# Performance work log

Measured on AMD Instinct MI355X. Metric: run time of the kernel, lower is better.

## Reference

```python
import jax, jax.numpy as jnp
import numpy as np

N, B, L, C, H = 16384, 16, 32, 256, 8
DH = C // H
K_STATIC = 16   # k_max for L=32 (L>20 -> min(16, L//2))
K_MIN = 8       # int(0.25*L)
LN_EPS = 1e-5


def _ln(x, g, b):
    m = x.mean(-1, keepdims=True)
    v = ((x - m) ** 2).mean(-1, keepdims=True)
    return (x - m) / jnp.sqrt(v + LN_EPS) * g + b


def setup_inputs() -> dict:
    key = jax.random.key(0)
    ks = jax.random.split(key, 12)
    s = 1.0 / np.sqrt(C)
    f32 = jnp.float32
    return {
        'vision_features': jax.random.normal(ks[0], (N, B, C), dtype=f32),
        'text_features': jax.random.normal(ks[1], (L, B, C), dtype=f32),
        'vp_w': jax.random.normal(ks[2], (C, C), dtype=f32) * s,
        'vp_b': jnp.zeros((C,), f32),
        'tp_w': jax.random.normal(ks[3], (C, C), dtype=f32) * s,
        'tp_b': jnp.zeros((C,), f32),
        'in_proj_w': jax.random.normal(ks[4], (3 * C, C), dtype=f32) * s,
        'in_proj_b': jnp.zeros((3 * C,), f32),
        'w1': jax.random.normal(ks[5], (C, C), dtype=f32) * s,
        'b1': jnp.zeros((C,), f32),
        'g1': jnp.ones((C,), f32),
        'be1': jnp.zeros((C,), f32),
        'w2': jax.random.normal(ks[6], (C // 2, C), dtype=f32) * s,
        'b2': jnp.zeros((C // 2,), f32),
        'g2': jnp.ones((C // 2,), f32),
        'be2': jnp.zeros((C // 2,), f32),
        'w3': jax.random.normal(ks[7], (1, C // 2), dtype=f32) * s,
        'b3': jnp.zeros((1,), f32),
        'k_weight': jnp.asarray(np.log(0.4 / 0.6), f32),
        'alpha_coarse': jnp.asarray(np.log(0.72 / 0.28), f32),
        'alpha_fine': jnp.asarray(np.log(0.82 / 0.18), f32),
    }


def reference(vision_features, text_features, vp_w, vp_b, tp_w, tp_b,
              in_proj_w, in_proj_b, w1, b1, g1, be1, w2, b2, g2, be2,
              w3, b3, k_weight, alpha_coarse, alpha_fine):
    # projections (torch Linear: y = x W^T + b)
    vision_proj = vision_features @ vp_w.T + vp_b  # [N,B,C]
    text_proj = text_features @ tp_w.T + tp_b      # [L,B,C]

    # nn.MultiheadAttention attention weights, averaged over heads
    qp = vision_proj @ in_proj_w[:C].T + in_proj_b[:C]
    kp = text_proj @ in_proj_w[C:2 * C].T + in_proj_b[C:2 * C]
    q = qp.reshape(N, B, H, DH)
    k = kp.reshape(L, B, H, DH)
    scores = jnp.einsum('nbhd,lbhd->bhnl', q, k) / np.sqrt(DH)
    attn = jax.nn.softmax(scores, axis=-1).mean(axis=1)  # [B,N,L]

    # data-dependent k_top per batch (unbiased variance over L, mean over N)
    mu = attn.mean(axis=-1, keepdims=True)
    var = ((attn - mu) ** 2).sum(axis=-1) / (L - 1)       # [B,N]
    attn_variance = var.mean(axis=1)                      # [B]
    k_ws = jax.nn.sigmoid(k_weight)
    ratio = jnp.clip(k_ws * (1.0 + attn_variance * 0.5), 0.25, 0.6)
    k_base = jnp.maximum(1, jnp.floor(L * ratio).astype(jnp.int32))
    k_top = jnp.maximum(K_MIN, jnp.minimum(jnp.minimum(K_STATIC, k_base), L))  # [B]

    # variable-k top-k via static K_STATIC + mask
    top = -jnp.sort(-attn, axis=-1)[..., :K_STATIC]       # [B,N,K]
    mask = jnp.arange(K_STATIC)[None, None, :] < k_top[:, None, None]
    logits = jnp.where(mask, top, -jnp.inf)
    w = jax.nn.softmax(logits, axis=-1)
    similarity_score = jnp.sum(jnp.where(mask, top * w, 0.0), axis=-1)  # [B,N]

    # importance MLP on raw vision features (dropout off at inference)
    h = jax.nn.relu(_ln(vision_features @ w1.T + b1, g1, be1))
    h = jax.nn.relu(_ln(h @ w2.T + b2, g2, be2))
    feature_importance = jax.nn.sigmoid(h @ w3.T + b3)[..., 0]  # [N,B]
    feature_importance = feature_importance.T                    # [B,N]

    def minmax(x):
        lo = x.min(axis=1, keepdims=True)
        rng = x.max(axis=1, keepdims=True) - lo
        return jnp.where(rng > 0, (x - lo) / rng, 0.0)

    sim_norm = minmax(similarity_score)
    imp_norm = minmax(feature_importance)

    alpha = (jax.nn.sigmoid(alpha_coarse) + jax.nn.sigmoid(alpha_fine)) / 2.0
    importance = alpha * sim_norm + (1.0 - alpha) * imp_norm  # [B,N]
    return importance.T  # [N,B]
```

## Files before the change

kernel.cpp:

```cpp
#include <hip/hip_runtime.h>
#include <hip/hip_bf16.h>

typedef _Float16 f16;
typedef _Float16 half8 __attribute__((ext_vector_type(8)));
typedef _Float16 half4 __attribute__((ext_vector_type(4)));
typedef float f32x4 __attribute__((ext_vector_type(4)));

typedef const __attribute__((address_space(1))) void gvoid;
typedef __attribute__((address_space(3))) void lvoid;
#define GLOAD16(src, dst) __builtin_amdgcn_global_load_lds((gvoid*)(src), (lvoid*)(dst), 16, 0, 0)

#define WQV_OFF   0u
#define WKT_OFF   262144u
#define KP_OFF    524288u
#define W2S_OFF   1048576u
#define SBIAS_OFF 3145728u
#define BQV_OFF   3162112u
#define BKT_OFF   3163136u
#define W1H_OFF   3164160u
#define W2H_OFF   3295232u
#define VARP_OFF  3360768u
#define SMM_OFF   3377280u
#define FMM_OFF   3377408u
#define CAND_OFF  3377664u
#define FI_OFF    12814848u
#define SIM_OFF   13863424u
#define XS_OFF    14912000u
#define XS_BYTES  134217728ull

__device__ __forceinline__ float sigm(float x) { return 1.f / (1.f + __expf(-x)); }
__device__ __forceinline__ unsigned fmap(float f) {
  unsigned u = __float_as_uint(f);
  return (u & 0x80000000u) ? ~u : (u | 0x80000000u);
}
__device__ __forceinline__ float funmap(unsigned u) {
  unsigned b = (u & 0x80000000u) ? (u & 0x7FFFFFFFu) : ~u;
  return __uint_as_float(b);
}

__global__ void k_p1(const float* __restrict__ ipw, const float* __restrict__ ipb,
                     const float* __restrict__ vp_w, const float* __restrict__ vp_b,
                     const float* __restrict__ tp_w, const float* __restrict__ tp_b,
                     float* __restrict__ Wqv, float* __restrict__ Wkt,
                     float* __restrict__ bqv, float* __restrict__ bkt,
                     unsigned* __restrict__ simMM, unsigned* __restrict__ fiMM) {
  int tx = threadIdx.x, ty = threadIdx.y;
  int bz = blockIdx.z;
  if (bz == 2) {
    if (blockIdx.x || blockIdx.y) return;
    if (ty == 0 && tx < 16) {
      simMM[tx * 2] = 0xFFFFFFFFu; simMM[tx * 2 + 1] = 0u;
      fiMM[tx * 2] = 0xFFFFFFFFu;  fiMM[tx * 2 + 1] = 0u;
    }
    int j = ty * 16 + tx;
    float s1 = 0.f, s2 = 0.f;
    for (int k = 0; k < 256; ++k) {
      s1 += ipw[j * 256 + k] * vp_b[k];
      s2 += ipw[65536 + j * 256 + k] * tp_b[k];
    }
    bqv[j] = s1 + ipb[j];
    bkt[j] = s2 + ipb[256 + j];
    return;
  }
  const float* A = ipw + (bz ? 65536 : 0);
  const float* B = bz ? tp_w : vp_w;
  float* O = bz ? Wkt : Wqv;
  __shared__ float As[16][16], Bs[16][17];
  int row = blockIdx.y * 16 + ty, col = blockIdx.x * 16 + tx;
  float s = 0.f;
  for (int tt = 0; tt < 16; ++tt) {
    As[ty][tx] = A[row * 256 + tt * 16 + tx];
    Bs[ty][tx] = B[(tt * 16 + ty) * 256 + col];
    __syncthreads();
#pragma unroll
    for (int k = 0; k < 16; ++k) s += As[ty][k] * Bs[k][tx];
    __syncthreads();
  }
  O[row * 256 + col] = s;
}

__global__ void k_conv(const float* __restrict__ w1, const float* __restrict__ w2,
                       char* __restrict__ W1g, char* __restrict__ W2g) {
  int i = blockIdx.x * 256 + threadIdx.x;
  if (i < 65536) {
    int o = i >> 8, c = i & 255;
    *(f16*)(W1g + (c >> 6) * 32768 + o * 128 + (((c & 63) << 1) ^ ((o & 7) << 4))) = (f16)w1[i];
  } else if (i < 98304) {
    int i2 = i - 65536;
    int o = i2 >> 8, c = i2 & 255;
    *(f16*)(W2g + (c >> 6) * 16384 + o * 128 + (((c & 63) << 1) ^ ((o & 7) << 4))) = (f16)w2[i2];
  }
}

__global__ void __launch_bounds__(256) k_tr(const float* __restrict__ X,
                                            char* __restrict__ XS) {
  int g0 = blockIdx.x * 256 + threadIdx.x;
#pragma unroll 4
  for (int i = 0; i < 16; ++i) {
    int G = g0 + i * 524288;
    int cg = G & 31;
    int nb = G >> 5;
    int b = nb & 15;
    int n = nb >> 4;
    f32x4 a0 = *(const f32x4*)(X + (size_t)G * 8);
    f32x4 a1 = *(const f32x4*)(X + (size_t)G * 8 + 4);
    half8 h;
#pragma unroll
    for (int j = 0; j < 4; ++j) { h[j] = (f16)a0[j]; h[4 + j] = (f16)a1[j]; }
    unsigned off = (unsigned)((cg >> 3) * 128 + (((cg & 7) << 4) ^ ((n & 7) << 4)));
    *(half8*)(XS + ((size_t)b * 16384 + n) * 512 + off) = h;
  }
}

__global__ void k_p2(const float* __restrict__ T, const float* __restrict__ Wkt,
                     const float* __restrict__ bkt, float* __restrict__ kp) {
  __shared__ float As[16][16], Ws[16][17];
  int tx = threadIdx.x, ty = threadIdx.y;
  int lb = blockIdx.y * 16 + ty;
  int i = blockIdx.x * 16 + tx;
  float s = 0.f;
  for (int tt = 0; tt < 16; ++tt) {
    As[ty][tx] = T[(size_t)lb * 256 + tt * 16 + tx];
    Ws[ty][tx] = Wkt[(size_t)(blockIdx.x * 16 + ty) * 256 + tt * 16 + tx];
    __syncthreads();
#pragma unroll
    for (int k = 0; k < 16; ++k) s += As[ty][k] * Ws[tx][k];
    __syncthreads();
  }
  kp[(size_t)lb * 256 + i] = s + bkt[i];
}

__global__ void k_p3(const float* __restrict__ kp, const float* __restrict__ Wqv,
                     const float* __restrict__ bqv, char* __restrict__ W2sg,
                     float* __restrict__ sbias) {
  const float SC = 0.17677669529663687f;
  int b = blockIdx.z, jt = blockIdx.y, ct = blockIdx.x;
  int ty = threadIdx.y, tx = threadIdx.x;
  int j2 = jt * 16 + ty, c = ct * 16 + tx;
  int h = j2 >> 5, l = j2 & 31;
  const float* kr = kp + (size_t)(l * 16 + b) * 256 + h * 32;
  const float* wq = Wqv + (size_t)h * 32 * 256 + c;
  float s = 0.f;
#pragma unroll
  for (int d = 0; d < 32; ++d) s += kr[d] * wq[(size_t)d * 256];
  *(f16*)(W2sg + (size_t)b * 131072 + (c >> 6) * 32768 + j2 * 128 +
          (((c & 63) << 1) ^ ((j2 & 7) << 4))) = (f16)(s * SC);
  if (ct == 0 && tx == 0) {
    float sb = 0.f;
#pragma unroll
    for (int d = 0; d < 32; ++d) sb += kr[d] * bqv[h * 32 + d];
    sbias[b * 256 + j2] = sb * SC;
  }
}

template <int CONT>
__global__ void __launch_bounds__(256, 3) k_sc(
    const float* __restrict__ X, const char* __restrict__ XSg,
    const char* __restrict__ W2sg, const float* __restrict__ sbias,
    float* __restrict__ cand, float* __restrict__ varpart) {
  __shared__ __align__(16) char smem[40960];
  const int b = blockIdx.y;
  const int bx = blockIdx.x;
  const int n0 = bx * 64;
  const int t = threadIdx.x;
  const int w = t >> 6;
  const int lane = t & 63;
  const int ln = lane & 15, kg = lane >> 4;
  char* AT = smem;
  char* BT = smem + 8192;
  const char* XSb = XSg + ((size_t)b * 16384 + n0) * 512;
  const char* Wb = W2sg + (size_t)b * 131072;

  auto issueA = [&](int kt) {
    if constexpr (CONT) {
      const char* src = XSb + (size_t)(w * 16 + (lane >> 3)) * 512 + kt * 128 + ((lane & 7) << 4);
      GLOAD16(src, AT + w * 2048);
      GLOAD16(src + 8 * 512, AT + w * 2048 + 1024);
    } else {
      int row = t >> 2, cq = t & 3;
      const float* Xr = X + ((size_t)(n0 + row) * 16 + b) * 256 + kt * 64 + cq * 16;
      f32x4 a0 = *(const f32x4*)(Xr), a1 = *(const f32x4*)(Xr + 4);
      f32x4 a2 = *(const f32x4*)(Xr + 8), a3 = *(const f32x4*)(Xr + 12);
      half8 h0, h1;
#pragma unroll
      for (int i = 0; i < 4; ++i) {
        h0[i] = (f16)a0[i]; h0[4 + i] = (f16)a1[i];
        h1[i] = (f16)a2[i]; h1[4 + i] = (f16)a3[i];
      }
      unsigned sw = (unsigned)((row & 7) << 4);
      *(half8*)(AT + ((unsigned)(row * 128 + cq * 32) ^ sw)) = h0;
      *(half8*)(AT + ((unsigned)(row * 128 + cq * 32 + 16) ^ sw)) = h1;
    }
  };
  auto issueB = [&](int kt) {
    const char* src = Wb + kt * 32768 + w * 8192 + (lane << 4);
    char* dst = BT + w * 8192;
#pragma unroll
    for (int i = 0; i < 8; ++i) GLOAD16(src + i * 1024, dst + i * 1024);
  };

  f32x4 acc[4][4];
#pragma unroll
  for (int q = 0; q < 4; ++q)
#pragma unroll
    for (int ni = 0; ni < 4; ++ni)
#pragma unroll
      for (int i = 0; i < 4; ++i) acc[q][ni][i] = 0.f;

  issueA(0); issueB(0);
  __syncthreads();
#pragma unroll
  for (int kt = 0; kt < 4; ++kt) {
    half8 av[4][2], bv[4][2];
#pragma unroll
    for (int q = 0; q < 4; ++q) {
      int o = w * 64 + q * 16 + ln;
      unsigned sw = (unsigned)((o & 7) << 4);
#pragma unroll
      for (int mi = 0; mi < 2; ++mi)
        av[q][mi] = *(const half8*)(BT + o * 128 + ((unsigned)(mi * 64 + kg * 16) ^ sw));
    }
#pragma unroll
    for (int ni = 0; ni < 4; ++ni) {
      int n = ni * 16 + ln;
      unsigned sw = (unsigned)((n & 7) << 4);
#pragma unroll
      for (int mi = 0; mi < 2; ++mi)
        bv[ni][mi] = *(const half8*)(AT + n * 128 + ((unsigned)(mi * 64 + kg * 16) ^ sw));
    }
#pragma unroll
    for (int mi = 0; mi < 2; ++mi)
#pragma unroll
      for (int q = 0; q < 4; ++q)
#pragma unroll
        for (int ni = 0; ni < 4; ++ni)
          acc[q][ni] = __builtin_amdgcn_mfma_f32_16x16x32_f16(av[q][mi], bv[ni][mi], acc[q][ni], 0, 0, 0);
    __syncthreads();
    if (kt < 3) { issueA(kt + 1); issueB(kt + 1); __syncthreads(); }
  }

  {
    f32x4 sb[4];
#pragma unroll
    for (int q = 0; q < 4; ++q)
      sb[q] = *(const f32x4*)(sbias + b * 256 + (w * 4 + q) * 16 + kg * 4);
    float vm[4][2][4];
#pragma unroll
    for (int ni = 0; ni < 4; ++ni)
#pragma unroll
      for (int qq = 0; qq < 2; ++qq)
#pragma unroll
        for (int r = 0; r < 4; ++r) vm[ni][qq][r] = 0.f;
#pragma unroll
    for (int hh = 0; hh < 2; ++hh)
#pragma unroll
      for (int ni = 0; ni < 4; ++ni) {
        float x[2][4];
        float mx = -1e30f;
#pragma unroll
        for (int qq = 0; qq < 2; ++qq)
#pragma unroll
          for (int r = 0; r < 4; ++r) {
            x[qq][r] = acc[hh * 2 + qq][ni][r] + sb[hh * 2 + qq][r];
            mx = fmaxf(mx, x[qq][r]);
          }
        mx = fmaxf(mx, __shfl_xor(mx, 16, 64));
        mx = fmaxf(mx, __shfl_xor(mx, 32, 64));
        float S = 0.f;
#pragma unroll
        for (int qq = 0; qq < 2; ++qq)
#pragma unroll
          for (int r = 0; r < 4; ++r) { x[qq][r] = __expf(x[qq][r] - mx); S += x[qq][r]; }
        S += __shfl_xor(S, 16, 64);
        S += __shfl_xor(S, 32, 64);
        float inv = 0.125f / S;
#pragma unroll
        for (int qq = 0; qq < 2; ++qq)
#pragma unroll
          for (int r = 0; r < 4; ++r) vm[ni][qq][r] += x[qq][r] * inv;
      }
    float* slice = (float*)(smem + 8192) + w * 2048;
#pragma unroll
    for (int ni = 0; ni < 4; ++ni)
#pragma unroll
      for (int qq = 0; qq < 2; ++qq)
#pragma unroll
        for (int r = 0; r < 4; ++r)
          slice[(qq * 16 + kg * 4 + r) * 64 + ni * 16 + ln] = vm[ni][qq][r];
  }
  __syncthreads();

  if (w == 0) {
    const float* sl = (const float*)(smem + 8192);
    float v[32];
#pragma unroll
    for (int l = 0; l < 32; ++l)
      v[l] = sl[l * 64 + lane] + sl[2048 + l * 64 + lane] +
             sl[4096 + l * 64 + lane] + sl[6144 + l * 64 + lane];
    float s2 = 0.f;
#pragma unroll
    for (int l = 0; l < 32; ++l) s2 += v[l] * v[l];
    float vr = (s2 - (1.f / 32.f)) * (1.f / 31.f);
#pragma unroll
    for (int m = 1; m < 64; m <<= 1) vr += __shfl_xor(vr, m, 64);
    if (lane == 0) varpart[b * 256 + bx] = vr;
#pragma unroll
    for (int k = 2; k <= 32; k <<= 1) {
#pragma unroll
      for (int j = k >> 1; j > 0; j >>= 1) {
#pragma unroll
        for (int i = 0; i < 32; ++i) {
          int l = i ^ j;
          if (l > i) {
            float a = v[i], c = v[l];
            float hi = fmaxf(a, c), lo = fminf(a, c);
            bool up = ((i & k) == 0);
            v[i] = up ? hi : lo;
            v[l] = up ? lo : hi;
          }
        }
      }
    }
    float m0 = v[0], se = 0.f, te = 0.f;
    float cn[9];
#pragma unroll
    for (int i = 0; i < 16; ++i) {
      float e = __expf(v[i] - m0);
      se += e; te += v[i] * e;
      if (i >= 7) cn[i - 7] = te / se;
    }
#pragma unroll
    for (int i = 0; i < 9; ++i)
      cand[(size_t)i * 262144 + (size_t)b * 16384 + n0 + lane] = cn[i];
  }
}

template <int CONT>
__global__ void __launch_bounds__(256, 3) k_mlp(
    const float* __restrict__ X, const char* __restrict__ XSg,
    const char* __restrict__ W1g, const char* __restrict__ W2g,
    const float* __restrict__ b1, const float* __restrict__ g1, const float* __restrict__ be1,
    const float* __restrict__ b2, const float* __restrict__ g2, const float* __restrict__ be2,
    const float* __restrict__ w3, const float* __restrict__ b3,
    float* __restrict__ fi) {
  __shared__ __align__(16) char smem[49152];
  __shared__ float pSQ[2][64][5];
  __shared__ float pM[64], pR[64];
  const int b = blockIdx.y;
  const int bx = blockIdx.x;
  const int n0 = bx * 64;
  const int t = threadIdx.x;
  const int w = t >> 6;
  const int lane = t & 63;
  const int ln = lane & 15, kg = lane >> 4;
  char* AT = smem;
  char* BT = smem + 8192;
  char* H1 = smem;
  char* W2T = smem + 32768;
  const char* XSb = XSg + ((size_t)b * 16384 + n0) * 512;

  auto issueA = [&](int kt) {
    if constexpr (CONT) {
      const char* src = XSb + (size_t)(w * 16 + (lane >> 3)) * 512 + kt * 128 + ((lane & 7) << 4);
      GLOAD16(src, AT + w * 2048);
      GLOAD16(src + 8 * 512, AT + w * 2048 + 1024);
    } else {
      int row = t >> 2, cq = t & 3;
      const float* Xr = X + ((size_t)(n0 + row) * 16 + b) * 256 + kt * 64 + cq * 16;
      f32x4 a0 = *(const f32x4*)(Xr), a1 = *(const f32x4*)(Xr + 4);
      f32x4 a2 = *(const f32x4*)(Xr + 8), a3 = *(const f32x4*)(Xr + 12);
      half8 h0, h1;
#pragma unroll
      for (int i = 0; i < 4; ++i) {
        h0[i] = (f16)a0[i]; h0[4 + i] = (f16)a1[i];
        h1[i] = (f16)a2[i]; h1[4 + i] = (f16)a3[i];
      }
      unsigned sw = (unsigned)((row & 7) << 4);
      *(half8*)(AT + ((unsigned)(row * 128 + cq * 32) ^ sw)) = h0;
      *(half8*)(AT + ((unsigned)(row * 128 + cq * 32 + 16) ^ sw)) = h1;
    }
  };
  auto issueB1 = [&](int kt) {
    const char* src = W1g + kt * 32768 + w * 8192 + (lane << 4);
    char* dst = BT + w * 8192;
#pragma unroll
    for (int i = 0; i < 8; ++i) GLOAD16(src + i * 1024, dst + i * 1024);
  };
  auto issueW2 = [&](int kt) {
    const char* src = W2g + kt * 16384 + w * 4096 + (lane << 4);
    char* dst = W2T + w * 4096;
    GLOAD16(src, dst);
    GLOAD16(src + 1024, dst + 1024);
    GLOAD16(src + 2048, dst + 2048);
    GLOAD16(src + 3072, dst + 3072);
  };

  f32x4 acc[4][4];
#pragma unroll
  for (int q = 0; q < 4; ++q)
#pragma unroll
    for (int ni = 0; ni < 4; ++ni)
#pragma unroll
      for (int i = 0; i < 4; ++i) acc[q][ni][i] = 0.f;

  issueA(0); issueB1(0);
  __syncthreads();
#pragma unroll
  for (int kt = 0; kt < 4; ++kt) {
    half8 av[4][2], bv[4][2];
#pragma unroll
    for (int q = 0; q < 4; ++q) {
      int o = w * 64 + q * 16 + ln;
      unsigned sw = (unsigned)((o & 7) << 4);
#pragma unroll
      for (int mi = 0; mi < 2; ++mi)
        av[q][mi] = *(const half8*)(BT + o * 128 + ((unsigned)(mi * 64 + kg * 16) ^ sw));
    }
#pragma unroll
    for (int ni = 0; ni < 4; ++ni) {
      int n = ni * 16 + ln;
      unsigned sw = (unsigned)((n & 7) << 4);
#pragma unroll
      for (int mi = 0; mi < 2; ++mi)
        bv[ni][mi] = *(const half8*)(AT + n * 128 + ((unsigned)(mi * 64 + kg * 16) ^ sw));
    }
#pragma unroll
    for (int mi = 0; mi < 2; ++mi)
#pragma unroll
      for (int q = 0; q < 4; ++q)
#pragma unroll
        for (int ni = 0; ni < 4; ++ni)
          acc[q][ni] = __builtin_amdgcn_mfma_f32_16x16x32_f16(av[q][mi], bv[ni][mi], acc[q][ni], 0, 0, 0);
    __syncthreads();
    if (kt < 3) { issueA(kt + 1); issueB1(kt + 1); __syncthreads(); }
  }
  issueW2(0);

  {
    f32x4 b1v[4];
#pragma unroll
    for (int q = 0; q < 4; ++q)
      b1v[q] = *(const f32x4*)(b1 + (w * 4 + q) * 16 + kg * 4);
#pragma unroll
    for (int ni = 0; ni < 4; ++ni) {
      float s = 0.f, qq = 0.f;
#pragma unroll
      for (int q = 0; q < 4; ++q)
#pragma unroll
        for (int r = 0; r < 4; ++r) {
          float v = acc[q][ni][r] + b1v[q][r];
          acc[q][ni][r] = v;
          s += v; qq += v * v;
        }
      s += __shfl_xor(s, 16, 64); s += __shfl_xor(s, 32, 64);
      qq += __shfl_xor(qq, 16, 64); qq += __shfl_xor(qq, 32, 64);
      if (kg == 0) { int n = ni * 16 + ln; pSQ[0][n][w] = s; pSQ[1][n][w] = qq; }
    }
  }
  __syncthreads();
  if (t < 64) {
    float s = pSQ[0][t][0] + pSQ[0][t][1] + pSQ[0][t][2] + pSQ[0][t][3];
    float q = pSQ[1][t][0] + pSQ[1][t][1] + pSQ[1][t][2] + pSQ[1][t][3];
    float mean = s * (1.f / 256.f);
    float var = q * (1.f / 256.f) - mean * mean;
    pM[t] = mean;
    pR[t] = rsqrtf(var + 1e-5f);
  }
  __syncthreads();

  {
    f32x4 g1v[4], e1v[4];
#pragma unroll
    for (int q = 0; q < 4; ++q) {
      g1v[q] = *(const f32x4*)(g1 + (w * 4 + q) * 16 + kg * 4);
      e1v[q] = *(const f32x4*)(be1 + (w * 4 + q) * 16 + kg * 4);
    }
#pragma unroll
    for (int ni = 0; ni < 4; ++ni) {
      int n = ni * 16 + ln;
      float mean = pM[n], rstd = pR[n];
      unsigned sw = (unsigned)((n & 7) << 4);
#pragma unroll
      for (int q = 0; q < 4; ++q) {
        half4 hv;
#pragma unroll
        for (int r = 0; r < 4; ++r) {
          float y = (acc[q][ni][r] - mean) * rstd * g1v[q][r] + e1v[q][r];
          hv[r] = (f16)fmaxf(y, 0.f);
        }
        *(half4*)(H1 + ((unsigned)(n * 512 + (w * 4 + q) * 32 + kg * 8) ^ sw)) = hv;
      }
    }
  }
  __syncthreads();

  f32x4 acc2[2][4];
#pragma unroll
  for (int oi = 0; oi < 2; ++oi)
#pragma unroll
    for (int ni = 0; ni < 4; ++ni)
#pragma unroll
      for (int i = 0; i < 4; ++i) acc2[oi][ni][i] = 0.f;
#pragma unroll
  for (int kt = 0; kt < 4; ++kt) {
    half8 a2[2][2], bv[4][2];
#pragma unroll
    for (int oi = 0; oi < 2; ++oi) {
      int o2 = w * 32 + oi * 16 + ln;
      unsigned sw = (unsigned)((o2 & 7) << 4);
#pragma unroll
      for (int mi = 0; mi < 2; ++mi)
        a2[oi][mi] = *(const half8*)(W2T + o2 * 128 + ((unsigned)(mi * 64 + kg * 16) ^ sw));
    }
#pragma unroll
    for (int ni = 0; ni < 4; ++ni) {
      int n = ni * 16 + ln;
      unsigned sw = (unsigned)((n & 7) << 4);
#pragma unroll
      for (int mi = 0; mi < 2; ++mi)
        bv[ni][mi] = *(const half8*)(H1 + n * 512 + kt * 128 + ((unsigned)(mi * 64 + kg * 16) ^ sw));
    }
#pragma unroll
    for (int mi = 0; mi < 2; ++mi)
#pragma unroll
      for (int oi = 0; oi < 2; ++oi)
#pragma unroll
        for (int ni = 0; ni < 4; ++ni)
          acc2[oi][ni] = __builtin_amdgcn_mfma_f32_16x16x32_f16(a2[oi][mi], bv[ni][mi], acc2[oi][ni], 0, 0, 0);
    __syncthreads();
    if (kt < 3) { issueW2(kt + 1); __syncthreads(); }
  }

  {
    f32x4 b2v[2], g2v[2], e2v[2], w3v[2];
#pragma unroll
    for (int oi = 0; oi < 2; ++oi) {
      b2v[oi] = *(const f32x4*)(b2 + (w * 2 + oi) * 16 + kg * 4);
      g2v[oi] = *(const f32x4*)(g2 + (w * 2 + oi) * 16 + kg * 4);
      e2v[oi] = *(const f32x4*)(be2 + (w * 2 + oi) * 16 + kg * 4);
      w3v[oi] = *(const f32x4*)(w3 + (w * 2 + oi) * 16 + kg * 4);
    }
#pragma unroll
    for (int ni = 0; ni < 4; ++ni) {
      float s = 0.f, q = 0.f;
#pragma unroll
      for (int oi = 0; oi < 2; ++oi)
#pragma unroll
        for (int r = 0; r < 4; ++r) {
          float v = acc2[oi][ni][r] + b2v[oi][r];
          acc2[oi][ni][r] = v;
          s += v; q += v * v;
        }
      s += __shfl_xor(s, 16, 64); s += __shfl_xor(s, 32, 64);
      q += __shfl_xor(q, 16, 64); q += __shfl_xor(q, 32, 64);
      if (kg == 0) { int n = ni * 16 + ln; pSQ[0][n][w] = s; pSQ[1][n][w] = q; }
    }
    __syncthreads();
    if (t < 64) {
      float s = pSQ[0][t][0] + pSQ[0][t][1] + pSQ[0][t][2] + pSQ[0][t][3];
      float q = pSQ[1][t][0] + pSQ[1][t][1] + pSQ[1][t][2] + pSQ[1][t][3];
      float mean = s * (1.f / 128.f);
      float var = q * (1.f / 128.f) - mean * mean;
      pM[t] = mean;
      pR[t] = rsqrtf(var + 1e-5f);
    }
    __syncthreads();
#pragma unroll
    for (int ni = 0; ni < 4; ++ni) {
      int n = ni * 16 + ln;
      float mean = pM[n], rstd = pR[n];
      float a3 = 0.f;
#pragma unroll
      for (int oi = 0; oi < 2; ++oi)
#pragma unroll
        for (int r = 0; r < 4; ++r) {
          float y = (acc2[oi][ni][r] - mean) * rstd * g2v[oi][r] + e2v[oi][r];
          a3 += fmaxf(y, 0.f) * w3v[oi][r];
        }
      a3 += __shfl_xor(a3, 16, 64);
      a3 += __shfl_xor(a3, 32, 64);
      if (kg == 0) pSQ[0][n][w] = a3;
    }
    __syncthreads();
    if (t < 64) {
      float z = pSQ[0][t][0] + pSQ[0][t][1] + pSQ[0][t][2] + pSQ[0][t][3] + b3[0];
      fi[(size_t)b * 16384 + n0 + t] = sigm(z);
    }
  }
}

__global__ void __launch_bounds__(256) k_g4(
    const float* __restrict__ cand, const float* __restrict__ fi,
    const float* __restrict__ varpart, const float* __restrict__ kw,
    float* __restrict__ sim, unsigned* __restrict__ simMM, unsigned* __restrict__ fiMM) {
  __shared__ float red[4][4];
  __shared__ int kS;
  int b = blockIdx.x >> 6;
  if (threadIdx.x < 64) {
    float s = 0.f;
#pragma unroll
    for (int i = 0; i < 4; ++i) s += varpart[b * 256 + threadIdx.x + i * 64];
#pragma unroll
    for (int m = 1; m < 64; m <<= 1) s += __shfl_xor(s, m, 64);
    if (threadIdx.x == 0) {
      float var = s * (1.f / 16384.f);
      float kws = sigm(kw[0]);
      float ratio = fminf(fmaxf(kws * (1.f + var * 0.5f), 0.25f), 0.6f);
      int kb = (int)floorf(32.f * ratio);
      if (kb < 1) kb = 1;
      int kt = kb < 16 ? kb : 16;
      if (kt < 8) kt = 8;
      kS = kt;
    }
  }
  __syncthreads();
  int k = kS;
  int n = (blockIdx.x & 63) * 256 + threadIdx.x;
  size_t idx = (size_t)b * 16384 + n;
  float sv = cand[(size_t)(k - 8) * 262144 + idx];
  sim[idx] = sv;
  float fv = fi[idx];
  float sn = sv, sx = sv, fn = fv, fx = fv;
#pragma unroll
  for (int m = 1; m < 64; m <<= 1) {
    sn = fminf(sn, __shfl_xor(sn, m, 64));
    sx = fmaxf(sx, __shfl_xor(sx, m, 64));
    fn = fminf(fn, __shfl_xor(fn, m, 64));
    fx = fmaxf(fx, __shfl_xor(fx, m, 64));
  }
  int wv = threadIdx.x >> 6;
  if ((threadIdx.x & 63) == 0) { red[0][wv] = sn; red[1][wv] = sx; red[2][wv] = fn; red[3][wv] = fx; }
  __syncthreads();
  if (threadIdx.x == 0) {
    float a = red[0][0], c = red[1][0], d = red[2][0], e = red[3][0];
#pragma unroll
    for (int i = 1; i < 4; ++i) {
      a = fminf(a, red[0][i]); c = fmaxf(c, red[1][i]);
      d = fminf(d, red[2][i]); e = fmaxf(e, red[3][i]);
    }
    atomicMin(&simMM[b * 2 + 0], fmap(a));
    atomicMax(&simMM[b * 2 + 1], fmap(c));
    atomicMin(&fiMM[b * 2 + 0], fmap(d));
    atomicMax(&fiMM[b * 2 + 1], fmap(e));
  }
}

__global__ void __launch_bounds__(256) k_g5(
    const float* __restrict__ sim, const float* __restrict__ fi,
    const unsigned* __restrict__ simMM, const unsigned* __restrict__ fiMM,
    const float* __restrict__ ac, const float* __restrict__ af,
    float* __restrict__ out) {
  __shared__ float ls[256][17], lf[256][17];
  __shared__ float sMin[16], sInv[16], fMin[16], fInv[16];
  int t = threadIdx.x;
  int n0 = blockIdx.x * 256;
  if (t < 16) {
    float lo = funmap(simMM[t * 2]), hi = funmap(simMM[t * 2 + 1]);
    float r = hi - lo;
    sMin[t] = lo; sInv[t] = (r > 0.f) ? 1.f / r : 0.f;
    lo = funmap(fiMM[t * 2]); hi = funmap(fiMM[t * 2 + 1]);
    r = hi - lo;
    fMin[t] = lo; fInv[t] = (r > 0.f) ? 1.f / r : 0.f;
  }
#pragma unroll
  for (int i = 0; i < 16; ++i) {
    ls[t][i] = sim[(size_t)i * 16384 + n0 + t];
    lf[t][i] = fi[(size_t)i * 16384 + n0 + t];
  }
  __syncthreads();
  float alpha = 0.5f * (sigm(ac[0]) + sigm(af[0]));
  float o[16];
#pragma unroll
  for (int b = 0; b < 16; ++b) {
    float s = (ls[t][b] - sMin[b]) * sInv[b];
    float f = (lf[t][b] - fMin[b]) * fInv[b];
    o[b] = alpha * s + (1.f - alpha) * f;
  }
  float* op = out + (size_t)(n0 + t) * 16;
#pragma unroll
  for (int i = 0; i < 4; ++i) {
    f32x4 v;
    v[0] = o[i * 4]; v[1] = o[i * 4 + 1]; v[2] = o[i * 4 + 2]; v[3] = o[i * 4 + 3];
    *(f32x4*)(op + i * 4) = v;
  }
}

extern "C" void kernel_launch(void* const* d_in, const int* in_sizes, int n_in,
                              void* d_out, int out_size, void* d_ws, size_t ws_size,
                              hipStream_t stream) {
  const float* X    = (const float*)d_in[0];
  const float* T    = (const float*)d_in[1];
  const float* vp_w = (const float*)d_in[2];
  const float* vp_b = (const float*)d_in[3];
  const float* tp_w = (const float*)d_in[4];
  const float* tp_b = (const float*)d_in[5];
  const float* ipw  = (const float*)d_in[6];
  const float* ipb  = (const float*)d_in[7];
  const float* w1   = (const float*)d_in[8];
  const float* b1   = (const float*)d_in[9];
  const float* g1   = (const float*)d_in[10];
  const float* be1  = (const float*)d_in[11];
  const float* w2   = (const float*)d_in[12];
  const float* b2   = (const float*)d_in[13];
  const float* g2   = (const float*)d_in[14];
  const float* be2  = (const float*)d_in[15];
  const float* w3   = (const float*)d_in[16];
  const float* b3   = (const float*)d_in[17];
  const float* kw   = (const float*)d_in[18];
  const float* ac   = (const float*)d_in[19];
  const float* af   = (const float*)d_in[20];
  char* ws = (char*)d_ws;
  float* Wqv = (float*)(ws + WQV_OFF);
  float* Wkt = (float*)(ws + WKT_OFF);
  float* kp = (float*)(ws + KP_OFF);
  char* W2sg = ws + W2S_OFF;
  float* sbias = (float*)(ws + SBIAS_OFF);
  float* bqv = (float*)(ws + BQV_OFF);
  float* bkt = (float*)(ws + BKT_OFF);
  char* W1g = ws + W1H_OFF;
  char* W2g = ws + W2H_OFF;
  float* varpart = (float*)(ws + VARP_OFF);
  unsigned* simMM = (unsigned*)(ws + SMM_OFF);
  unsigned* fiMM = (unsigned*)(ws + FMM_OFF);
  float* cand = (float*)(ws + CAND_OFF);
  float* fi = (float*)(ws + FI_OFF);
  float* sim = (float*)(ws + SIM_OFF);
  char* XS = ws + XS_OFF;
  float* out = (float*)d_out;

  const bool cont = (ws_size >= (size_t)XS_OFF + XS_BYTES);

  k_p1<<<dim3(16, 16, 3), dim3(16, 16), 0, stream>>>(ipw, ipb, vp_w, vp_b, tp_w, tp_b,
                                                     Wqv, Wkt, bqv, bkt, simMM, fiMM);
  k_conv<<<384, 256, 0, stream>>>(w1, w2, W1g, W2g);
  if (cont) k_tr<<<2048, 256, 0, stream>>>(X, XS);
  k_p2<<<dim3(16, 32), dim3(16, 16), 0, stream>>>(T, Wkt, bkt, kp);
  k_p3<<<dim3(16, 16, 16), dim3(16, 16), 0, stream>>>(kp, Wqv, bqv, W2sg, sbias);
  if (cont) {
    k_sc<1><<<dim3(256, 16), 256, 0, stream>>>(X, XS, W2sg, sbias, cand, varpart);
    k_mlp<1><<<dim3(256, 16), 256, 0, stream>>>(X, XS, W1g, W2g, b1, g1, be1,
                                                b2, g2, be2, w3, b3, fi);
  } else {
    k_sc<0><<<dim3(256, 16), 256, 0, stream>>>(X, XS, W2sg, sbias, cand, varpart);
    k_mlp<0><<<dim3(256, 16), 256, 0, stream>>>(X, XS, W1g, W2g, b1, g1, be1,
                                                b2, g2, be2, w3, b3, fi);
  }
  k_g4<<<1024, 256, 0, stream>>>(cand, fi, varpart, kw, sim, simMM, fiMM);
  k_g5<<<64, 256, 0, stream>>>(sim, fi, simMM, fiMM, ac, af, out);
}
```

Before: 305.2 us.

## Double-buffer LDS tiles in score and MLP GEMM kernels

Gives the K-loop tile buffers in k_sc and k_mlp, including the W2 tiles of the second MLP GEMM, two LDS slots. The next tile's global-to-LDS loads are issued before the current tile is read, which removes the extra barrier per iteration and overlaps memory with MFMA work. The cost is doubled LDS use, 80 KB per block, so launch bounds drop from 3 to 2 blocks per CU. The LN reduction scratch moves into the shared buffer. Lower occupancy may offset the gain from overlap.

```diff
diff --git a/kernel.cpp b/kernel.cpp
--- a/kernel.cpp
+++ b/kernel.cpp
@@ -154,11 +154,11 @@
 }
 
 template <int CONT>
-__global__ void __launch_bounds__(256, 3) k_sc(
+__global__ void __launch_bounds__(256, 2) k_sc(
     const float* __restrict__ X, const char* __restrict__ XSg,
     const char* __restrict__ W2sg, const float* __restrict__ sbias,
     float* __restrict__ cand, float* __restrict__ varpart) {
-  __shared__ __align__(16) char smem[40960];
+  __shared__ __align__(16) char smem[81920];
   const int b = blockIdx.y;
   const int bx = blockIdx.x;
   const int n0 = bx * 64;
@@ -166,16 +166,15 @@
   const int w = t >> 6;
   const int lane = t & 63;
   const int ln = lane & 15, kg = lane >> 4;
-  char* AT = smem;
-  char* BT = smem + 8192;
   const char* XSb = XSg + ((size_t)b * 16384 + n0) * 512;
   const char* Wb = W2sg + (size_t)b * 131072;
 
-  auto issueA = [&](int kt) {
+  auto issueA = [&](int kt, int p) {
+    char* ATp = smem + p * 8192;
     if constexpr (CONT) {
       const char* src = XSb + (size_t)(w * 16 + (lane >> 3)) * 512 + kt * 128 + ((lane & 7) << 4);
-      GLOAD16(src, AT + w * 2048);
-      GLOAD16(src + 8 * 512, AT + w * 2048 + 1024);
+      GLOAD16(src, ATp + w * 2048);
+      GLOAD16(src + 8 * 512, ATp + w * 2048 + 1024);
     } else {
       int row = t >> 2, cq = t & 3;
       const float* Xr = X + ((size_t)(n0 + row) * 16 + b) * 256 + kt * 64 + cq * 16;
@@ -188,13 +187,13 @@
         h1[i] = (f16)a2[i]; h1[4 + i] = (f16)a3[i];
       }
       unsigned sw = (unsigned)((row & 7) << 4);
-      *(half8*)(AT + ((unsigned)(row * 128 + cq * 32) ^ sw)) = h0;
-      *(half8*)(AT + ((unsigned)(row * 128 + cq * 32 + 16) ^ sw)) = h1;
+      *(half8*)(ATp + ((unsigned)(row * 128 + cq * 32) ^ sw)) = h0;
+      *(half8*)(ATp + ((unsigned)(row * 128 + cq * 32 + 16) ^ sw)) = h1;
     }
   };
-  auto issueB = [&](int kt) {
+  auto issueB = [&](int kt, int p) {
     const char* src = Wb + kt * 32768 + w * 8192 + (lane << 4);
-    char* dst = BT + w * 8192;
+    char* dst = smem + 16384 + p * 32768 + w * 8192;
 #pragma unroll
     for (int i = 0; i < 8; ++i) GLOAD16(src + i * 1024, dst + i * 1024);
   };
@@ -207,10 +206,14 @@
 #pragma unroll
       for (int i = 0; i < 4; ++i) acc[q][ni][i] = 0.f;
 
-  issueA(0); issueB(0);
+  issueA(0, 0); issueB(0, 0);
   __syncthreads();
 #pragma unroll
   for (int kt = 0; kt < 4; ++kt) {
+    const int p = kt & 1;
+    if (kt < 3) { issueA(kt + 1, p ^ 1); issueB(kt + 1, p ^ 1); }
+    char* ATp = smem + p * 8192;
+    char* BTp = smem + 16384 + p * 32768;
     half8 av[4][2], bv[4][2];
 #pragma unroll
     for (int q = 0; q < 4; ++q) {
@@ -218,7 +221,7 @@
       unsigned sw = (unsigned)((o & 7) << 4);
 #pragma unroll
       for (int mi = 0; mi < 2; ++mi)
-        av[q][mi] = *(const half8*)(BT + o * 128 + ((unsigned)(mi * 64 + kg * 16) ^ sw));
+        av[q][mi] = *(const half8*)(BTp + o * 128 + ((unsigned)(mi * 64 + kg * 16) ^ sw));
     }
 #pragma unroll
     for (int ni = 0; ni < 4; ++ni) {
@@ -226,7 +229,7 @@
       unsigned sw = (unsigned)((n & 7) << 4);
 #pragma unroll
       for (int mi = 0; mi < 2; ++mi)
-        bv[ni][mi] = *(const half8*)(AT + n * 128 + ((unsigned)(mi * 64 + kg * 16) ^ sw));
+        bv[ni][mi] = *(const half8*)(ATp + n * 128 + ((unsigned)(mi * 64 + kg * 16) ^ sw));
     }
 #pragma unroll
     for (int mi = 0; mi < 2; ++mi)
@@ -236,7 +239,6 @@
         for (int ni = 0; ni < 4; ++ni)
           acc[q][ni] = __builtin_amdgcn_mfma_f32_16x16x32_f16(av[q][mi], bv[ni][mi], acc[q][ni], 0, 0, 0);
     __syncthreads();
-    if (kt < 3) { issueA(kt + 1); issueB(kt + 1); __syncthreads(); }
   }
 
   {
@@ -279,7 +281,7 @@
 #pragma unroll
           for (int r = 0; r < 4; ++r) vm[ni][qq][r] += x[qq][r] * inv;
       }
-    float* slice = (float*)(smem + 8192) + w * 2048;
+    float* slice = (float*)(smem + 16384) + w * 2048;
 #pragma unroll
     for (int ni = 0; ni < 4; ++ni)
 #pragma unroll
@@ -291,7 +293,7 @@
   __syncthreads();
 
   if (w == 0) {
-    const float* sl = (const float*)(smem + 8192);
+    const float* sl = (const float*)(smem + 16384);
     float v[32];
 #pragma unroll
     for (int l = 0; l < 32; ++l)
@@ -336,16 +338,18 @@
 }
 
 template <int CONT>
-__global__ void __launch_bounds__(256, 3) k_mlp(
+__global__ void __launch_bounds__(256, 2) k_mlp(
     const float* __restrict__ X, const char* __restrict__ XSg,
     const char* __restrict__ W1g, const char* __restrict__ W2g,
     const float* __restrict__ b1, const float* __restrict__ g1, const float* __restrict__ be1,
     const float* __restrict__ b2, const float* __restrict__ g2, const float* __restrict__ be2,
     const float* __restrict__ w3, const float* __restrict__ b3,
     float* __restrict__ fi) {
-  __shared__ __align__(16) char smem[49152];
-  __shared__ float pSQ[2][64][5];
-  __shared__ float pM[64], pR[64];
+  __shared__ __align__(16) char smem[81920];
+  float* pS = (float*)(smem + 65536);
+  float* pQ = (float*)(smem + 66816);
+  float* pM = (float*)(smem + 68096);
+  float* pR = (float*)(smem + 68352);
   const int b = blockIdx.y;
   const int bx = blockIdx.x;
   const int n0 = bx * 64;
@@ -353,17 +357,15 @@
   const int w = t >> 6;
   const int lane = t & 63;
   const int ln = lane & 15, kg = lane >> 4;
-  char* AT = smem;
-  char* BT = smem + 8192;
   char* H1 = smem;
-  char* W2T = smem + 32768;
   const char* XSb = XSg + ((size_t)b * 16384 + n0) * 512;
 
-  auto issueA = [&](int kt) {
+  auto issueA = [&](int kt, int p) {
+    char* ATp = smem + p * 8192;
     if constexpr (CONT) {
       const char* src = XSb + (size_t)(w * 16 + (lane >> 3)) * 512 + kt * 128 + ((lane & 7) << 4);
-      GLOAD16(src, AT + w * 2048);
-      GLOAD16(src + 8 * 512, AT + w * 2048 + 1024);
+      GLOAD16(src, ATp + w * 2048);
+      GLOAD16(src + 8 * 512, ATp + w * 2048 + 1024);
     } else {
       int row = t >> 2, cq = t & 3;
       const float* Xr = X + ((size_t)(n0 + row) * 16 + b) * 256 + kt * 64 + cq * 16;
@@ -376,19 +378,19 @@
         h1[i] = (f16)a2[i]; h1[4 + i] = (f16)a3[i];
       }
       unsigned sw = (unsigned)((row & 7) << 4);
-      *(half8*)(AT + ((unsigned)(row * 128 + cq * 32) ^ sw)) = h0;
-      *(half8*)(AT + ((unsigned)(row * 128 + cq * 32 + 16) ^ sw)) = h1;
+      *(half8*)(ATp + ((unsigned)(row * 128 + cq * 32) ^ sw)) = h0;
+      *(half8*)(ATp + ((unsigned)(row * 128 + cq * 32 + 16) ^ sw)) = h1;
     }
   };
-  auto issueB1 = [&](int kt) {
+  auto issueB1 = [&](int kt, int p) {
     const char* src = W1g + kt * 32768 + w * 8192 + (lane << 4);
-    char* dst = BT + w * 8192;
+    char* dst = smem + 16384 + p * 32768 + w * 8192;
 #pragma unroll
     for (int i = 0; i < 8; ++i) GLOAD16(src + i * 1024, dst + i * 1024);
   };
-  auto issueW2 = [&](int kt) {
+  auto issueW2 = [&](int kt, int p) {
     const char* src = W2g + kt * 16384 + w * 4096 + (lane << 4);
-    char* dst = W2T + w * 4096;
+    char* dst = smem + 32768 + p * 16384 + w * 4096;
     GLOAD16(src, dst);
     GLOAD16(src + 1024, dst + 1024);
     GLOAD16(src + 2048, dst + 2048);
@@ -403,10 +405,14 @@
 #pragma unroll
       for (int i = 0; i < 4; ++i) acc[q][ni][i] = 0.f;
 
-  issueA(0); issueB1(0);
+  issueA(0, 0); issueB1(0, 0);
   __syncthreads();
 #pragma unroll
   for (int kt = 0; kt < 4; ++kt) {
+    const int p = kt & 1;
+    if (kt < 3) { issueA(kt + 1, p ^ 1); issueB1(kt + 1, p ^ 1); }
+    char* ATp = smem + p * 8192;
+    char* BTp = smem + 16384 + p * 32768;
     half8 av[4][2], bv[4][2];
 #pragma unroll
     for (int q = 0; q < 4; ++q) {
@@ -414,7 +420,7 @@
       unsigned sw = (unsigned)((o & 7) << 4);
 #pragma unroll
       for (int mi = 0; mi < 2; ++mi)
-        av[q][mi] = *(const half8*)(BT + o * 128 + ((unsigned)(mi * 64 + kg * 16) ^ sw));
+        av[q][mi] = *(const half8*)(BTp + o * 128 + ((unsigned)(mi * 64 + kg * 16) ^ sw));
     }
 #pragma unroll
     for (int ni = 0; ni < 4; ++ni) {
@@ -422,7 +428,7 @@
       unsigned sw = (unsigned)((n & 7) << 4);
 #pragma unroll
       for (int mi = 0; mi < 2; ++mi)
-        bv[ni][mi] = *(const half8*)(AT + n * 128 + ((unsigned)(mi * 64 + kg * 16) ^ sw));
+        bv[ni][mi] = *(const half8*)(ATp + n * 128 + ((unsigned)(mi * 64 + kg * 16) ^ sw));
     }
 #pragma unroll
     for (int mi = 0; mi < 2; ++mi)
@@ -432,9 +438,7 @@
         for (int ni = 0; ni < 4; ++ni)
           acc[q][ni] = __builtin_amdgcn_mfma_f32_16x16x32_f16(av[q][mi], bv[ni][mi], acc[q][ni], 0, 0, 0);
     __syncthreads();
-    if (kt < 3) { issueA(kt + 1); issueB1(kt + 1); __syncthreads(); }
-  }
-  issueW2(0);
+  }
 
   {
     f32x4 b1v[4];
@@ -454,13 +458,13 @@
         }
       s += __shfl_xor(s, 16, 64); s += __shfl_xor(s, 32, 64);
       qq += __shfl_xor(qq, 16, 64); qq += __shfl_xor(qq, 32, 64);
-      if (kg == 0) { int n = ni * 16 + ln; pSQ[0][n][w] = s; pSQ[1][n][w] = qq; }
+      if (kg == 0) { int n = ni * 16 + ln; pS[n * 5 + w] = s; pQ[n * 5 + w] = qq; }
     }
   }
   __syncthreads();
   if (t < 64) {
-    float s = pSQ[0][t][0] + pSQ[0][t][1] + pSQ[0][t][2] + pSQ[0][t][3];
-    float q = pSQ[1][t][0] + pSQ[1][t][1] + pSQ[1][t][2] + pSQ[1][t][3];
+    float s = pS[t * 5 + 0] + pS[t * 5 + 1] + pS[t * 5 + 2] + pS[t * 5 + 3];
+    float q = pQ[t * 5 + 0] + pQ[t * 5 + 1] + pQ[t * 5 + 2] + pQ[t * 5 + 3];
     float mean = s * (1.f / 256.f);
     float var = q * (1.f / 256.f) - mean * mean;
     pM[t] = mean;
@@ -468,6 +472,7 @@
   }
   __syncthreads();
 
+  issueW2(0, 0);
   {
     f32x4 g1v[4], e1v[4];
 #pragma unroll
@@ -503,6 +508,9 @@
       for (int i = 0; i < 4; ++i) acc2[oi][ni][i] = 0.f;
 #pragma unroll
   for (int kt = 0; kt < 4; ++kt) {
+    const int p = kt & 1;
+    if (kt < 3) issueW2(kt + 1, p ^ 1);
+    char* W2Tp = smem + 32768 + p * 16384;
     half8 a2[2][2], bv[4][2];
 #pragma unroll
     for (int oi = 0; oi < 2; ++oi) {
@@ -510,7 +518,7 @@
       unsigned sw = (unsigned)((o2 & 7) << 4);
 #pragma unroll
       for (int mi = 0; mi < 2; ++mi)
-        a2[oi][mi] = *(const half8*)(W2T + o2 * 128 + ((unsigned)(mi * 64 + kg * 16) ^ sw));
+        a2[oi][mi] = *(const half8*)(W2Tp + o2 * 128 + ((unsigned)(mi * 64 + kg * 16) ^ sw));
     }
 #pragma unroll
     for (int ni = 0; ni < 4; ++ni) {
@@ -528,7 +536,6 @@
         for (int ni = 0; ni < 4; ++ni)
           acc2[oi][ni] = __builtin_amdgcn_mfma_f32_16x16x32_f16(a2[oi][mi], bv[ni][mi], acc2[oi][ni], 0, 0, 0);
     __syncthreads();
-    if (kt < 3) { issueW2(kt + 1); __syncthreads(); }
   }
 
   {
@@ -553,12 +560,12 @@
         }
       s += __shfl_xor(s, 16, 64); s += __shfl_xor(s, 32, 64);
       q += __shfl_xor(q, 16, 64); q += __shfl_xor(q, 32, 64);
-      if (kg == 0) { int n = ni * 16 + ln; pSQ[0][n][w] = s; pSQ[1][n][w] = q; }
+      if (kg == 0) { int n = ni * 16 + ln; pS[n * 5 + w] = s; pQ[n * 5 + w] = q; }
     }
     __syncthreads();
     if (t < 64) {
-      float s = pSQ[0][t][0] + pSQ[0][t][1] + pSQ[0][t][2] + pSQ[0][t][3];
-      float q = pSQ[1][t][0] + pSQ[1][t][1] + pSQ[1][t][2] + pSQ[1][t][3];
+      float s = pS[t * 5 + 0] + pS[t * 5 + 1] + pS[t * 5 + 2] + pS[t * 5 + 3];
+      float q = pQ[t * 5 + 0] + pQ[t * 5 + 1] + pQ[t * 5 + 2] + pQ[t * 5 + 3];
       float mean = s * (1.f / 128.f);
       float var = q * (1.f / 128.f) - mean * mean;
       pM[t] = mean;
@@ -579,11 +586,11 @@
         }
       a3 += __shfl_xor(a3, 16, 64);
       a3 += __shfl_xor(a3, 32, 64);
-      if (kg == 0) pSQ[0][n][w] = a3;
+      if (kg == 0) pS[n * 5 + w] = a3;
     }
     __syncthreads();
     if (t < 64) {
-      float z = pSQ[0][t][0] + pSQ[0][t][1] + pSQ[0][t][2] + pSQ[0][t][3] + b3[0];
+      float z = pS[t * 5 + 0] + pS[t * 5 + 1] + pS[t * 5 + 2] + pS[t * 5 + 3] + b3[0];
       fi[(size_t)b * 16384 + n0 + t] = sigm(z);
     }
   }
```

New measurement: 335.7 us. +10.0%, slower.
